# Optimization experiments

Measured on AMD Instinct MI355X. Metric: run time of the kernel, lower is better.

## Reference

```python
import jax, jax.numpy as jnp
import numpy as np

THRESHOLD = 0.1  # init kwarg threshold
N_HITS_PER_EVENT = 200000
N_EVENTS = 64


def setup_inputs() -> dict:
    key = jax.random.key(0)
    n = N_HITS_PER_EVENT * N_EVENTS
    score = jax.random.uniform(key, (n, 1), dtype=jnp.float32)  # noise score in (0,1)
    row_splits = (jnp.arange(N_EVENTS + 1, dtype=jnp.int32) * N_HITS_PER_EVENT)
    return {"score": score, "row_splits": row_splits}


def reference(score, row_splits):
    """Faithful, fully vectorized version of select_threshold_with_backgather.

    Per segment: keep all vertices with score > threshold PLUS all vertices tied
    with the segment minimum score; non-kept vertices backgather to the FIRST
    kept minimum-score vertex of their segment (new/compacted indexing).
    Returns (sel [M,1], newrs [n_seg+1], backgather [N,1]) in the layer's
    call-output order (sel, newrs, allbackgather).
    """
    s = score[:, 0]
    n = s.shape[0]
    n_seg = row_splits.shape[0] - 1

    # segment id of every vertex from the row splits
    segids = jnp.searchsorted(row_splits, jnp.arange(n, dtype=row_splits.dtype), side='right') - 1
    segids = segids.astype(jnp.int32)

    # per-segment minimum score; ties with the min are all kept (== original isminscore)
    segmin = jax.ops.segment_min(s, segids, num_segments=n_seg)
    ismin = s == segmin[segids]
    keep = (s > THRESHOLD) | ismin

    # global compacted position of each kept vertex (n_previous_rs + local keeprange)
    kept_pos = jnp.cumsum(keep.astype(jnp.int32)) - 1

    # representative = first kept min-score vertex per segment (original minidx + n_previous_rs)
    big = jnp.int32(n)
    rep_pos = jax.ops.segment_min(jnp.where(keep & ismin, kept_pos, big), segids, num_segments=n_seg)

    backgather = jnp.where(keep, kept_pos, rep_pos[segids])

    # selection indices (data-dependent size; computed on concrete values, not under jit)
    sel = jnp.nonzero(keep)[0].astype(jnp.int32)

    counts = jax.ops.segment_sum(keep.astype(jnp.int32), segids, num_segments=n_seg)
    newrs = jnp.concatenate([jnp.zeros((1,), jnp.int32), jnp.cumsum(counts).astype(jnp.int32)])

    return sel[:, None], newrs, backgather[:, None].astype(jnp.int32)
```

## Files before the change

### kernel.cpp

```cpp
#include <hip/hip_runtime.h>
#include <stdint.h>

#define BLOCK 256
#define ITEMS 8
#define TILE (BLOCK * ITEMS)
#define WPB (TILE / 64)
#define MAXSEG 64
#define THRESH 0.1f

typedef unsigned long long u64;

__device__ __forceinline__ int find_seg(const int* rs, int n_seg, int i) {
    int lo = 0, hi = n_seg;
    while (hi - lo > 1) {
        int mid = (lo + hi) >> 1;
        if (rs[mid] <= i) lo = mid; else hi = mid;
    }
    return lo;
}

__global__ __launch_bounds__(BLOCK) void k_pass1(const float* __restrict__ score,
        const int* __restrict__ row_splits, int n_seg, int n, int nwords,
        u64* __restrict__ partial_val, int* __restrict__ partial_seg,
        u64* __restrict__ bitmask, int* __restrict__ block_counts) {
    __shared__ int rs[MAXSEG + 1];
    __shared__ u64 wval[8];
    __shared__ int wseg[8];
    __shared__ int wsum[4];
    for (int j = threadIdx.x; j <= n_seg; j += BLOCK) rs[j] = row_splits[j];
    __syncthreads();
    int lane = threadIdx.x & 63, wv = threadIdx.x >> 6;
    int wbase = blockIdx.x * TILE + wv * 512;
    u64 m0 = ~0ull, m1 = ~0ull;
    int sf = -1, sl = -1, cnt = 0;
    if (wbase < n) {
        int wend = min(n, wbase + 512) - 1;
        sf = find_seg(rs, n_seg, wbase);
        sl = find_seg(rs, n_seg, wend);
        int bval = (sl != sf) ? rs[sf + 1] : 0x7FFFFFFF;
        int tbase = wbase + lane * 8;
        unsigned int kbyte = 0;
        if (tbase < n) {
            float v[8];
            if (tbase + 8 <= n) {
                float4 f0 = *(const float4*)(score + tbase);
                float4 f1 = *(const float4*)(score + tbase + 4);
                v[0]=f0.x; v[1]=f0.y; v[2]=f0.z; v[3]=f0.w;
                v[4]=f1.x; v[5]=f1.y; v[6]=f1.z; v[7]=f1.w;
            } else {
                for (int j = 0; j < 8; j++) v[j] = (tbase + j < n) ? score[tbase + j] : 1.0f;
            }
            #pragma unroll
            for (int j = 0; j < 8; j++) {
                int i = tbase + j;
                if (i < n) {
                    u64 p = ((u64)__float_as_uint(v[j]) << 32) | (unsigned int)i;
                    if (i < bval) m0 = min(m0, p); else m1 = min(m1, p);
                    if (v[j] > THRESH) kbyte |= 1u << j;
                }
            }
            cnt = __popc(kbyte);
        }
        u64 acc = ((u64)kbyte) << (8 * (lane & 7));
        acc |= __shfl_xor((unsigned long long)acc, 1, 64);
        acc |= __shfl_xor((unsigned long long)acc, 2, 64);
        acc |= __shfl_xor((unsigned long long)acc, 4, 64);
        int src = (lane < 8) ? (8 * lane) : lane;
        u64 myword = __shfl((unsigned long long)acc, src, 64);
        for (int o = 32; o > 0; o >>= 1) {
            m0 = min(m0, (u64)__shfl_down((unsigned long long)m0, o, 64));
            m1 = min(m1, (u64)__shfl_down((unsigned long long)m1, o, 64));
            cnt += __shfl_down(cnt, o, 64);
        }
        if (lane < 8) {
            int w = (wbase >> 6) + lane;
            if (w < nwords) bitmask[w] = myword;
        }
    }
    if (lane == 0) {
        wval[2 * wv] = m0;     wseg[2 * wv] = sf;
        wval[2 * wv + 1] = m1; wseg[2 * wv + 1] = (sl != sf) ? sl : -1;
        wsum[wv] = (wbase < n) ? cnt : 0;
    }
    __syncthreads();
    if (threadIdx.x == 0) {
        int base = blockIdx.x * TILE;
        int endi = min(n, base + TILE) - 1;
        int s0 = find_seg(rs, n_seg, base);
        int s1 = find_seg(rs, n_seg, endi);
        u64 o0 = ~0ull, o1 = ~0ull;
        for (int k = 0; k < 8; k++) {
            if (wseg[k] == s0) o0 = min(o0, wval[k]);
            else if (wseg[k] == s1) o1 = min(o1, wval[k]);
        }
        partial_val[2 * blockIdx.x] = o0;
        partial_seg[2 * blockIdx.x] = s0;
        partial_val[2 * blockIdx.x + 1] = o1;
        partial_seg[2 * blockIdx.x + 1] = (s1 != s0) ? s1 : -1;
        block_counts[blockIdx.x] = wsum[0] + wsum[1] + wsum[2] + wsum[3];
    }
}

__global__ __launch_bounds__(BLOCK) void k_segfix(const float* __restrict__ score,
        const int* __restrict__ row_splits, int n_seg, int n,
        const u64* __restrict__ partial_val, const int* __restrict__ partial_seg,
        u64* __restrict__ seg_packed, u64* __restrict__ bitmask,
        int* __restrict__ block_counts) {
    __shared__ u64 wred[4];
    __shared__ int nmatch;
    __shared__ int mlist[64];
    int s = blockIdx.x;
    int lo = row_splits[s], hi = row_splits[s + 1];
    int lane = threadIdx.x & 63, wv = threadIdx.x >> 6;
    if (threadIdx.x == 0) nmatch = 0;
    u64 m = ~0ull;
    int e0 = 0, e1 = -1;
    if (hi > lo) {
        e0 = 2 * (lo / TILE);
        e1 = 2 * ((hi - 1) / TILE) + 1;
        for (int e = e0 + threadIdx.x; e <= e1; e += BLOCK)
            if (partial_seg[e] == s) m = min(m, partial_val[e]);
    }
    for (int o = 32; o > 0; o >>= 1)
        m = min(m, (u64)__shfl_down((unsigned long long)m, o, 64));
    if (lane == 0) wred[wv] = m;
    __syncthreads();
    if (threadIdx.x == 0) {
        u64 r = min(min(wred[0], wred[1]), min(wred[2], wred[3]));
        wred[0] = r;
        seg_packed[s] = r;
    }
    __syncthreads();
    u64 sp = wred[0];
    if (sp == ~0ull) return;
    unsigned int smb = (unsigned int)(sp >> 32);
    if (__uint_as_float(smb) > THRESH) return;
    for (int e = e0 + threadIdx.x; e <= e1; e += BLOCK) {
        if (partial_seg[e] == s && (unsigned int)(partial_val[e] >> 32) == smb) {
            int k = atomicAdd(&nmatch, 1);
            if (k < 64) mlist[k] = e >> 1;
        }
    }
    __syncthreads();
    int nm = min(nmatch, 64);
    for (int k = 0; k < nm; k++) {
        int b = mlist[k];
        int rlo = max(b * TILE, lo);
        int rhi = min(min((b + 1) * TILE, n), hi);
        int c = 0;
        for (int i = rlo + threadIdx.x; i < rhi; i += BLOCK) {
            if (__float_as_uint(score[i]) == smb) {
                atomicOr(&bitmask[i >> 6], 1ull << (i & 63));
                c++;
            }
        }
        for (int o = 32; o > 0; o >>= 1) c += __shfl_down(c, o, 64);
        if (lane == 0 && c) atomicAdd(&block_counts[b], c);
    }
}

__global__ __launch_bounds__(BLOCK) void k_scanq(const int* __restrict__ counts,
        int* __restrict__ offsets, int nb,
        const int* __restrict__ row_splits, int n_seg, int n, int M,
        const u64* __restrict__ seg_packed, const u64* __restrict__ bitmask,
        int* __restrict__ rep_pos, int* __restrict__ newrs_out) {
    __shared__ int wtot[BLOCK / 64];
    int lane = threadIdx.x & 63, wv = threadIdx.x >> 6;
    {
        int per = (nb + BLOCK - 1) / BLOCK;
        int s = per * threadIdx.x, e = min(nb, s + per);
        int sum = 0;
        for (int i = s; i < e; i++) sum += counts[i];
        int incl = sum;
        for (int o = 1; o < 64; o <<= 1) {
            int t = __shfl_up(incl, o, 64);
            if (lane >= o) incl += t;
        }
        if (lane == 63) wtot[wv] = incl;
        __syncthreads();
        int excl = incl - sum;
        for (int k = 0; k < wv; k++) excl += wtot[k];
        for (int i = s; i < e; i++) { offsets[i] = excl; excl += counts[i]; }
    }
    __syncthreads();
    int nq = 2 * n_seg + 1;
    int q = threadIdx.x;
    if (q < nq) {
        unsigned int uidx;
        if (q <= n_seg) uidx = (unsigned int)row_splits[q];
        else uidx = (unsigned int)(seg_packed[q - (n_seg + 1)] & 0xFFFFFFFFu);
        int result;
        if (uidx >= (unsigned int)n) {
            result = M;
        } else {
            int idx = (int)uidx;
            int b = idx / TILE;
            int wq = idx >> 6;
            int cnt = offsets[b];
            for (int w = b * WPB; w < wq; w++) cnt += __popcll(bitmask[w]);
            if (idx & 63) cnt += __popcll(bitmask[wq] & ((1ull << (idx & 63)) - 1));
            result = cnt;
        }
        if (q <= n_seg) newrs_out[q] = result;
        else rep_pos[q - (n_seg + 1)] = result;
    }
}

__global__ __launch_bounds__(BLOCK) void k_output(const int* __restrict__ row_splits,
        int n_seg, int n,
        const int* __restrict__ rep_pos, const u64* __restrict__ bitmask,
        const int* __restrict__ block_offsets,
        int* __restrict__ sel_out, int* __restrict__ back_out) {
    __shared__ int rs[MAXSEG + 1];
    __shared__ u64 swords[WPB];
    __shared__ int wpre[WPB];
    __shared__ int shead[6];
    __shared__ alignas(16) int skel[TILE + 8];
    for (int j = threadIdx.x; j <= n_seg; j += BLOCK) rs[j] = row_splits[j];
    int base = blockIdx.x * TILE;
    int lim = min(TILE, n - base);
    int nw = (lim + 63) >> 6;
    for (int j = threadIdx.x; j < nw; j += BLOCK) swords[j] = bitmask[(base >> 6) + j];
    __syncthreads();
    if (threadIdx.x == 0) {
        int acc = 0;
        for (int k = 0; k < nw; k++) { wpre[k] = acc; acc += __popcll(swords[k]); }
        int s0 = find_seg(rs, n_seg, base);
        int s1 = find_seg(rs, n_seg, base + lim - 1);
        shead[0] = (s1 != s0) ? rs[s0 + 1] : 0x7FFFFFFF;
        shead[1] = rep_pos[s0];
        shead[2] = rep_pos[s1];
        shead[3] = acc;
    }
    __syncthreads();
    int bval = shead[0], rep0 = shead[1], rep1 = shead[2], tot = shead[3];
    int bo = block_offsets[blockIdx.x];
    int st_b = (int)((4 - ((((uintptr_t)(back_out + base)) >> 2) & 3)) & 3);
    if (st_b > lim) st_b = lim;
    int st_s = (int)((4 - ((((uintptr_t)(sel_out + bo)) >> 2) & 3)) & 3);
    if (st_s > tot) st_s = tot;
    int selpad = 4 - st_s;

    int ngroups = (lim - st_b) >> 2;
    for (int g = threadIdx.x; g < ngroups; g += BLOCK) {
        int j0 = st_b + 4 * g;
        int vals[4];
        #pragma unroll
        for (int k = 0; k < 4; k++) {
            int j = j0 + k;
            int widx = j >> 6, r = j & 63;
            u64 w = swords[widx];
            int i = base + j;
            if ((w >> r) & 1) {
                int pos = bo + wpre[widx] + __popcll(w & ((1ull << r) - 1));
                vals[k] = pos;
                skel[pos - bo + selpad] = i;
            } else {
                vals[k] = (i >= bval) ? rep1 : rep0;
            }
        }
        *(int4*)(back_out + base + j0) = make_int4(vals[0], vals[1], vals[2], vals[3]);
    }
    for (int j = threadIdx.x; j < st_b; j += BLOCK) {
        int widx = j >> 6, r = j & 63;
        u64 w = swords[widx];
        int i = base + j, val;
        if ((w >> r) & 1) {
            int pos = bo + wpre[widx] + __popcll(w & ((1ull << r) - 1));
            val = pos;
            skel[pos - bo + selpad] = i;
        } else val = (i >= bval) ? rep1 : rep0;
        back_out[i] = val;
    }
    for (int j = st_b + 4 * ngroups + threadIdx.x; j < lim; j += BLOCK) {
        int widx = j >> 6, r = j & 63;
        u64 w = swords[widx];
        int i = base + j, val;
        if ((w >> r) & 1) {
            int pos = bo + wpre[widx] + __popcll(w & ((1ull << r) - 1));
            val = pos;
            skel[pos - bo + selpad] = i;
        } else val = (i >= bval) ? rep1 : rep0;
        back_out[i] = val;
    }
    __syncthreads();
    int nvg = (tot - st_s) >> 2;
    for (int g = threadIdx.x; g < nvg; g += BLOCK) {
        int4 v = *(const int4*)&skel[4 + 4 * g];
        *(int4*)(sel_out + bo + st_s + 4 * g) = v;
    }
    for (int j = threadIdx.x; j < st_s; j += BLOCK) sel_out[bo + j] = skel[j + selpad];
    for (int j = st_s + 4 * nvg + threadIdx.x; j < tot; j += BLOCK) sel_out[bo + j] = skel[j + selpad];
}

extern "C" void kernel_launch(void* const* d_in, const int* in_sizes, int n_in,
                              void* d_out, int out_size, void* d_ws, size_t ws_size,
                              hipStream_t stream) {
    const float* score = (const float*)d_in[0];
    const int* row_splits = (const int*)d_in[1];
    int n = in_sizes[0];
    int n_seg = in_sizes[1] - 1;
    int M = out_size - (n_seg + 1) - n;
    int nb = (n + TILE - 1) / TILE;
    int nwords = (n + 63) / 64;

    u64* seg_packed   = (u64*)d_ws;
    u64* partial_val  = seg_packed + MAXSEG;
    int* partial_seg  = (int*)(partial_val + 2 * nb);
    int* rep_pos      = partial_seg + 2 * nb;
    int* block_counts = rep_pos + 64;
    int* block_offsets= block_counts + nb;
    uintptr_t bm_addr = (uintptr_t)(block_offsets + nb);
    bm_addr = (bm_addr + 7) & ~(uintptr_t)7;
    u64* bitmask      = (u64*)bm_addr;

    int* out = (int*)d_out;
    int* sel_out   = out;
    int* newrs_out = out + M;
    int* back_out  = out + M + (n_seg + 1);

    hipLaunchKernelGGL(k_pass1, dim3(nb), dim3(BLOCK), 0, stream,
                       score, row_splits, n_seg, n, nwords,
                       partial_val, partial_seg, bitmask, block_counts);
    hipLaunchKernelGGL(k_segfix, dim3(n_seg), dim3(BLOCK), 0, stream,
                       score, row_splits, n_seg, n,
                       partial_val, partial_seg, seg_packed, bitmask, block_counts);
    hipLaunchKernelGGL(k_scanq, dim3(1), dim3(BLOCK), 0, stream,
                       block_counts, block_offsets, nb,
                       row_splits, n_seg, n, M, seg_packed, bitmask,
                       rep_pos, newrs_out);
    hipLaunchKernelGGL(k_output, dim3(nb), dim3(BLOCK), 0, stream,
                       row_splits, n_seg, n, rep_pos, bitmask,
                       block_offsets, sel_out, back_out);
}
```

Before: 173.6 us.

## Fuse four kernels into one persistent cooperative kernel with grid syncs

```diff
diff --git a/kernel.cpp b/kernel.cpp
--- a/kernel.cpp
+++ b/kernel.cpp
@@ -1,12 +1,15 @@
 #include <hip/hip_runtime.h>
+#include <hip/hip_cooperative_groups.h>
 #include <stdint.h>
 
+namespace cg = cooperative_groups;
+
 #define BLOCK 256
-#define ITEMS 8
-#define TILE (BLOCK * ITEMS)
+#define TILE 2048
 #define WPB (TILE / 64)
 #define MAXSEG 64
 #define THRESH 0.1f
+#define GRID 512
 
 typedef unsigned long long u64;
 
@@ -19,278 +22,280 @@
     return lo;
 }
 
-__global__ __launch_bounds__(BLOCK) void k_pass1(const float* __restrict__ score,
-        const int* __restrict__ row_splits, int n_seg, int n, int nwords,
+__global__ __launch_bounds__(BLOCK, 2) void k_fused(
+        const float* __restrict__ score, const int* __restrict__ row_splits,
+        int n_seg, int n, int nb, int nwords, int M,
         u64* __restrict__ partial_val, int* __restrict__ partial_seg,
-        u64* __restrict__ bitmask, int* __restrict__ block_counts) {
+        u64* __restrict__ seg_packed, u64* __restrict__ bitmask,
+        int* __restrict__ block_counts, int* __restrict__ block_offsets,
+        int* __restrict__ rep_pos, int* __restrict__ sel_out,
+        int* __restrict__ newrs_out, int* __restrict__ back_out) {
+    cg::grid_group grid = cg::this_grid();
     __shared__ int rs[MAXSEG + 1];
     __shared__ u64 wval[8];
     __shared__ int wseg[8];
     __shared__ int wsum[4];
-    for (int j = threadIdx.x; j <= n_seg; j += BLOCK) rs[j] = row_splits[j];
-    __syncthreads();
-    int lane = threadIdx.x & 63, wv = threadIdx.x >> 6;
-    int wbase = blockIdx.x * TILE + wv * 512;
-    u64 m0 = ~0ull, m1 = ~0ull;
-    int sf = -1, sl = -1, cnt = 0;
-    if (wbase < n) {
-        int wend = min(n, wbase + 512) - 1;
-        sf = find_seg(rs, n_seg, wbase);
-        sl = find_seg(rs, n_seg, wend);
-        int bval = (sl != sf) ? rs[sf + 1] : 0x7FFFFFFF;
-        int tbase = wbase + lane * 8;
-        unsigned int kbyte = 0;
-        if (tbase < n) {
-            float v[8];
-            if (tbase + 8 <= n) {
-                float4 f0 = *(const float4*)(score + tbase);
-                float4 f1 = *(const float4*)(score + tbase + 4);
-                v[0]=f0.x; v[1]=f0.y; v[2]=f0.z; v[3]=f0.w;
-                v[4]=f1.x; v[5]=f1.y; v[6]=f1.z; v[7]=f1.w;
-            } else {
-                for (int j = 0; j < 8; j++) v[j] = (tbase + j < n) ? score[tbase + j] : 1.0f;
-            }
-            #pragma unroll
-            for (int j = 0; j < 8; j++) {
-                int i = tbase + j;
-                if (i < n) {
-                    u64 p = ((u64)__float_as_uint(v[j]) << 32) | (unsigned int)i;
-                    if (i < bval) m0 = min(m0, p); else m1 = min(m1, p);
-                    if (v[j] > THRESH) kbyte |= 1u << j;
-                }
-            }
-            cnt = __popc(kbyte);
-        }
-        u64 acc = ((u64)kbyte) << (8 * (lane & 7));
-        acc |= __shfl_xor((unsigned long long)acc, 1, 64);
-        acc |= __shfl_xor((unsigned long long)acc, 2, 64);
-        acc |= __shfl_xor((unsigned long long)acc, 4, 64);
-        int src = (lane < 8) ? (8 * lane) : lane;
-        u64 myword = __shfl((unsigned long long)acc, src, 64);
-        for (int o = 32; o > 0; o >>= 1) {
-            m0 = min(m0, (u64)__shfl_down((unsigned long long)m0, o, 64));
-            m1 = min(m1, (u64)__shfl_down((unsigned long long)m1, o, 64));
-            cnt += __shfl_down(cnt, o, 64);
-        }
-        if (lane < 8) {
-            int w = (wbase >> 6) + lane;
-            if (w < nwords) bitmask[w] = myword;
-        }
-    }
-    if (lane == 0) {
-        wval[2 * wv] = m0;     wseg[2 * wv] = sf;
-        wval[2 * wv + 1] = m1; wseg[2 * wv + 1] = (sl != sf) ? sl : -1;
-        wsum[wv] = (wbase < n) ? cnt : 0;
-    }
-    __syncthreads();
-    if (threadIdx.x == 0) {
-        int base = blockIdx.x * TILE;
-        int endi = min(n, base + TILE) - 1;
-        int s0 = find_seg(rs, n_seg, base);
-        int s1 = find_seg(rs, n_seg, endi);
-        u64 o0 = ~0ull, o1 = ~0ull;
-        for (int k = 0; k < 8; k++) {
-            if (wseg[k] == s0) o0 = min(o0, wval[k]);
-            else if (wseg[k] == s1) o1 = min(o1, wval[k]);
-        }
-        partial_val[2 * blockIdx.x] = o0;
-        partial_seg[2 * blockIdx.x] = s0;
-        partial_val[2 * blockIdx.x + 1] = o1;
-        partial_seg[2 * blockIdx.x + 1] = (s1 != s0) ? s1 : -1;
-        block_counts[blockIdx.x] = wsum[0] + wsum[1] + wsum[2] + wsum[3];
-    }
-}
-
-__global__ __launch_bounds__(BLOCK) void k_segfix(const float* __restrict__ score,
-        const int* __restrict__ row_splits, int n_seg, int n,
-        const u64* __restrict__ partial_val, const int* __restrict__ partial_seg,
-        u64* __restrict__ seg_packed, u64* __restrict__ bitmask,
-        int* __restrict__ block_counts) {
     __shared__ u64 wred[4];
     __shared__ int nmatch;
     __shared__ int mlist[64];
-    int s = blockIdx.x;
-    int lo = row_splits[s], hi = row_splits[s + 1];
+    __shared__ int wtot[4];
+    __shared__ u64 swords[WPB];
+    __shared__ int wpre[WPB];
+    __shared__ int shead[4];
+    __shared__ int srep[MAXSEG];
+    __shared__ alignas(16) int skel[TILE + 8];
+
+    int bid = blockIdx.x;
     int lane = threadIdx.x & 63, wv = threadIdx.x >> 6;
-    if (threadIdx.x == 0) nmatch = 0;
-    u64 m = ~0ull;
-    int e0 = 0, e1 = -1;
-    if (hi > lo) {
-        e0 = 2 * (lo / TILE);
-        e1 = 2 * ((hi - 1) / TILE) + 1;
-        for (int e = e0 + threadIdx.x; e <= e1; e += BLOCK)
-            if (partial_seg[e] == s) m = min(m, partial_val[e]);
-    }
-    for (int o = 32; o > 0; o >>= 1)
-        m = min(m, (u64)__shfl_down((unsigned long long)m, o, 64));
-    if (lane == 0) wred[wv] = m;
+    for (int j = threadIdx.x; j <= n_seg; j += BLOCK) rs[j] = row_splits[j];
     __syncthreads();
-    if (threadIdx.x == 0) {
-        u64 r = min(min(wred[0], wred[1]), min(wred[2], wred[3]));
-        wred[0] = r;
-        seg_packed[s] = r;
-    }
-    __syncthreads();
-    u64 sp = wred[0];
-    if (sp == ~0ull) return;
-    unsigned int smb = (unsigned int)(sp >> 32);
-    if (__uint_as_float(smb) > THRESH) return;
-    for (int e = e0 + threadIdx.x; e <= e1; e += BLOCK) {
-        if (partial_seg[e] == s && (unsigned int)(partial_val[e] >> 32) == smb) {
-            int k = atomicAdd(&nmatch, 1);
-            if (k < 64) mlist[k] = e >> 1;
-        }
-    }
-    __syncthreads();
-    int nm = min(nmatch, 64);
-    for (int k = 0; k < nm; k++) {
-        int b = mlist[k];
-        int rlo = max(b * TILE, lo);
-        int rhi = min(min((b + 1) * TILE, n), hi);
-        int c = 0;
-        for (int i = rlo + threadIdx.x; i < rhi; i += BLOCK) {
-            if (__float_as_uint(score[i]) == smb) {
-                atomicOr(&bitmask[i >> 6], 1ull << (i & 63));
-                c++;
-            }
-        }
-        for (int o = 32; o > 0; o >>= 1) c += __shfl_down(c, o, 64);
-        if (lane == 0 && c) atomicAdd(&block_counts[b], c);
-    }
-}
-
-__global__ __launch_bounds__(BLOCK) void k_scanq(const int* __restrict__ counts,
-        int* __restrict__ offsets, int nb,
-        const int* __restrict__ row_splits, int n_seg, int n, int M,
-        const u64* __restrict__ seg_packed, const u64* __restrict__ bitmask,
-        int* __restrict__ rep_pos, int* __restrict__ newrs_out) {
-    __shared__ int wtot[BLOCK / 64];
-    int lane = threadIdx.x & 63, wv = threadIdx.x >> 6;
-    {
+
+    for (int t = bid; t < nb; t += GRID) {
+        int wbase = t * TILE + wv * 512;
+        u64 m0 = ~0ull, m1 = ~0ull;
+        int sf = -1, sl = -1, cnt = 0;
+        if (wbase < n) {
+            int wend = min(n, wbase + 512) - 1;
+            sf = find_seg(rs, n_seg, wbase);
+            sl = find_seg(rs, n_seg, wend);
+            int bval = (sl != sf) ? rs[sf + 1] : 0x7FFFFFFF;
+            int tbase = wbase + lane * 8;
+            unsigned int kbyte = 0;
+            if (tbase < n) {
+                float v[8];
+                if (tbase + 8 <= n) {
+                    float4 f0 = *(const float4*)(score + tbase);
+                    float4 f1 = *(const float4*)(score + tbase + 4);
+                    v[0]=f0.x; v[1]=f0.y; v[2]=f0.z; v[3]=f0.w;
+                    v[4]=f1.x; v[5]=f1.y; v[6]=f1.z; v[7]=f1.w;
+                } else {
+                    for (int j = 0; j < 8; j++) v[j] = (tbase + j < n) ? score[tbase + j] : 1.0f;
+                }
+                #pragma unroll
+                for (int j = 0; j < 8; j++) {
+                    int i = tbase + j;
+                    if (i < n) {
+                        u64 p = ((u64)__float_as_uint(v[j]) << 32) | (unsigned int)i;
+                        if (i < bval) m0 = min(m0, p); else m1 = min(m1, p);
+                        if (v[j] > THRESH) kbyte |= 1u << j;
+                    }
+                }
+                cnt = __popc(kbyte);
+            }
+            u64 acc = ((u64)kbyte) << (8 * (lane & 7));
+            acc |= __shfl_xor((unsigned long long)acc, 1, 64);
+            acc |= __shfl_xor((unsigned long long)acc, 2, 64);
+            acc |= __shfl_xor((unsigned long long)acc, 4, 64);
+            int src = (lane < 8) ? (8 * lane) : lane;
+            u64 myword = __shfl((unsigned long long)acc, src, 64);
+            for (int o = 32; o > 0; o >>= 1) {
+                m0 = min(m0, (u64)__shfl_down((unsigned long long)m0, o, 64));
+                m1 = min(m1, (u64)__shfl_down((unsigned long long)m1, o, 64));
+                cnt += __shfl_down(cnt, o, 64);
+            }
+            if (lane < 8) {
+                int w = (wbase >> 6) + lane;
+                if (w < nwords) bitmask[w] = myword;
+            }
+        }
+        if (lane == 0) {
+            wval[2 * wv] = m0;     wseg[2 * wv] = sf;
+            wval[2 * wv + 1] = m1; wseg[2 * wv + 1] = (sl != sf) ? sl : -1;
+            wsum[wv] = (wbase < n) ? cnt : 0;
+        }
+        __syncthreads();
+        if (threadIdx.x == 0) {
+            int base = t * TILE;
+            int endi = min(n, base + TILE) - 1;
+            int s0 = find_seg(rs, n_seg, base);
+            int s1 = find_seg(rs, n_seg, endi);
+            u64 o0 = ~0ull, o1 = ~0ull;
+            for (int k = 0; k < 8; k++) {
+                if (wseg[k] == s0) o0 = min(o0, wval[k]);
+                else if (wseg[k] == s1) o1 = min(o1, wval[k]);
+            }
+            partial_val[2 * t] = o0;
+            partial_seg[2 * t] = s0;
+            partial_val[2 * t + 1] = o1;
+            partial_seg[2 * t + 1] = (s1 != s0) ? s1 : -1;
+            block_counts[t] = wsum[0] + wsum[1] + wsum[2] + wsum[3];
+        }
+        __syncthreads();
+    }
+    grid.sync();
+
+    if (bid < n_seg) {
+        int s = bid;
+        int lo = rs[s], hi = rs[s + 1];
+        if (threadIdx.x == 0) nmatch = 0;
+        u64 m = ~0ull;
+        int e0 = 0, e1 = -1;
+        if (hi > lo) {
+            e0 = 2 * (lo / TILE);
+            e1 = 2 * ((hi - 1) / TILE) + 1;
+            for (int e = e0 + threadIdx.x; e <= e1; e += BLOCK)
+                if (partial_seg[e] == s) m = min(m, partial_val[e]);
+        }
+        for (int o = 32; o > 0; o >>= 1)
+            m = min(m, (u64)__shfl_down((unsigned long long)m, o, 64));
+        if (lane == 0) wred[wv] = m;
+        __syncthreads();
+        if (threadIdx.x == 0) {
+            u64 r = min(min(wred[0], wred[1]), min(wred[2], wred[3]));
+            wred[0] = r;
+            seg_packed[s] = r;
+        }
+        __syncthreads();
+        u64 sp = wred[0];
+        bool doit = (sp != ~0ull) &&
+                    (__uint_as_float((unsigned int)(sp >> 32)) <= THRESH);
+        if (doit) {
+            unsigned int smb = (unsigned int)(sp >> 32);
+            for (int e = e0 + threadIdx.x; e <= e1; e += BLOCK) {
+                if (partial_seg[e] == s && (unsigned int)(partial_val[e] >> 32) == smb) {
+                    int k = atomicAdd(&nmatch, 1);
+                    if (k < 64) mlist[k] = e >> 1;
+                }
+            }
+            __syncthreads();
+            int nm = min(nmatch, 64);
+            for (int k = 0; k < nm; k++) {
+                int b = mlist[k];
+                int rlo = max(b * TILE, lo);
+                int rhi = min(min((b + 1) * TILE, n), hi);
+                int c = 0;
+                for (int i = rlo + threadIdx.x; i < rhi; i += BLOCK) {
+                    if (__float_as_uint(score[i]) == smb) {
+                        atomicOr(&bitmask[i >> 6], 1ull << (i & 63));
+                        c++;
+                    }
+                }
+                for (int o = 32; o > 0; o >>= 1) c += __shfl_down(c, o, 64);
+                if (lane == 0 && c) atomicAdd(&block_counts[b], c);
+            }
+        }
+    }
+    grid.sync();
+
+    if (bid == 0) {
         int per = (nb + BLOCK - 1) / BLOCK;
-        int s = per * threadIdx.x, e = min(nb, s + per);
+        int s0 = per * threadIdx.x, e0i = min(nb, s0 + per);
         int sum = 0;
-        for (int i = s; i < e; i++) sum += counts[i];
+        for (int i = s0; i < e0i; i++) sum += block_counts[i];
         int incl = sum;
         for (int o = 1; o < 64; o <<= 1) {
-            int t = __shfl_up(incl, o, 64);
-            if (lane >= o) incl += t;
+            int tsh = __shfl_up(incl, o, 64);
+            if (lane >= o) incl += tsh;
         }
         if (lane == 63) wtot[wv] = incl;
         __syncthreads();
         int excl = incl - sum;
         for (int k = 0; k < wv; k++) excl += wtot[k];
-        for (int i = s; i < e; i++) { offsets[i] = excl; excl += counts[i]; }
-    }
+        for (int i = s0; i < e0i; i++) { block_offsets[i] = excl; excl += block_counts[i]; }
+        __syncthreads();
+        int nq = 2 * n_seg + 1;
+        int q = threadIdx.x;
+        if (q < nq) {
+            unsigned int uidx;
+            if (q <= n_seg) uidx = (unsigned int)rs[q];
+            else uidx = (unsigned int)(seg_packed[q - (n_seg + 1)] & 0xFFFFFFFFu);
+            int result;
+            if (uidx >= (unsigned int)n) {
+                result = M;
+            } else {
+                int idx = (int)uidx;
+                int b = idx / TILE;
+                int wq = idx >> 6;
+                int cnt = block_offsets[b];
+                for (int w = b * WPB; w < wq; w++) cnt += __popcll(bitmask[w]);
+                if (idx & 63) cnt += __popcll(bitmask[wq] & ((1ull << (idx & 63)) - 1));
+                result = cnt;
+            }
+            if (q <= n_seg) newrs_out[q] = result;
+            else rep_pos[q - (n_seg + 1)] = result;
+        }
+    }
+    grid.sync();
+
+    for (int j = threadIdx.x; j < n_seg; j += BLOCK) srep[j] = rep_pos[j];
     __syncthreads();
-    int nq = 2 * n_seg + 1;
-    int q = threadIdx.x;
-    if (q < nq) {
-        unsigned int uidx;
-        if (q <= n_seg) uidx = (unsigned int)row_splits[q];
-        else uidx = (unsigned int)(seg_packed[q - (n_seg + 1)] & 0xFFFFFFFFu);
-        int result;
-        if (uidx >= (unsigned int)n) {
-            result = M;
-        } else {
-            int idx = (int)uidx;
-            int b = idx / TILE;
-            int wq = idx >> 6;
-            int cnt = offsets[b];
-            for (int w = b * WPB; w < wq; w++) cnt += __popcll(bitmask[w]);
-            if (idx & 63) cnt += __popcll(bitmask[wq] & ((1ull << (idx & 63)) - 1));
-            result = cnt;
-        }
-        if (q <= n_seg) newrs_out[q] = result;
-        else rep_pos[q - (n_seg + 1)] = result;
-    }
-}
-
-__global__ __launch_bounds__(BLOCK) void k_output(const int* __restrict__ row_splits,
-        int n_seg, int n,
-        const int* __restrict__ rep_pos, const u64* __restrict__ bitmask,
-        const int* __restrict__ block_offsets,
-        int* __restrict__ sel_out, int* __restrict__ back_out) {
-    __shared__ int rs[MAXSEG + 1];
-    __shared__ u64 swords[WPB];
-    __shared__ int wpre[WPB];
-    __shared__ int shead[6];
-    __shared__ alignas(16) int skel[TILE + 8];
-    for (int j = threadIdx.x; j <= n_seg; j += BLOCK) rs[j] = row_splits[j];
-    int base = blockIdx.x * TILE;
-    int lim = min(TILE, n - base);
-    int nw = (lim + 63) >> 6;
-    for (int j = threadIdx.x; j < nw; j += BLOCK) swords[j] = bitmask[(base >> 6) + j];
-    __syncthreads();
-    if (threadIdx.x == 0) {
-        int acc = 0;
-        for (int k = 0; k < nw; k++) { wpre[k] = acc; acc += __popcll(swords[k]); }
-        int s0 = find_seg(rs, n_seg, base);
-        int s1 = find_seg(rs, n_seg, base + lim - 1);
-        shead[0] = (s1 != s0) ? rs[s0 + 1] : 0x7FFFFFFF;
-        shead[1] = rep_pos[s0];
-        shead[2] = rep_pos[s1];
-        shead[3] = acc;
-    }
-    __syncthreads();
-    int bval = shead[0], rep0 = shead[1], rep1 = shead[2], tot = shead[3];
-    int bo = block_offsets[blockIdx.x];
-    int st_b = (int)((4 - ((((uintptr_t)(back_out + base)) >> 2) & 3)) & 3);
-    if (st_b > lim) st_b = lim;
-    int st_s = (int)((4 - ((((uintptr_t)(sel_out + bo)) >> 2) & 3)) & 3);
-    if (st_s > tot) st_s = tot;
-    int selpad = 4 - st_s;
-
-    int ngroups = (lim - st_b) >> 2;
-    for (int g = threadIdx.x; g < ngroups; g += BLOCK) {
-        int j0 = st_b + 4 * g;
-        int vals[4];
-        #pragma unroll
-        for (int k = 0; k < 4; k++) {
-            int j = j0 + k;
+    for (int t = bid; t < nb; t += GRID) {
+        int base = t * TILE;
+        int lim = min(TILE, n - base);
+        int nw = (lim + 63) >> 6;
+        for (int j = threadIdx.x; j < nw; j += BLOCK) swords[j] = bitmask[(base >> 6) + j];
+        __syncthreads();
+        if (threadIdx.x == 0) {
+            int acc = 0;
+            for (int k = 0; k < nw; k++) { wpre[k] = acc; acc += __popcll(swords[k]); }
+            int s0 = find_seg(rs, n_seg, base);
+            int s1 = find_seg(rs, n_seg, base + lim - 1);
+            shead[0] = (s1 != s0) ? rs[s0 + 1] : 0x7FFFFFFF;
+            shead[1] = srep[s0];
+            shead[2] = srep[s1];
+            shead[3] = acc;
+        }
+        __syncthreads();
+        int bval = shead[0], rep0 = shead[1], rep1 = shead[2], tot = shead[3];
+        int bo = block_offsets[t];
+        int st_b = (int)((4 - ((((uintptr_t)(back_out + base)) >> 2) & 3)) & 3);
+        if (st_b > lim) st_b = lim;
+        int st_s = (int)((4 - ((((uintptr_t)(sel_out + bo)) >> 2) & 3)) & 3);
+        if (st_s > tot) st_s = tot;
+        int selpad = 4 - st_s;
+
+        int ngroups = (lim - st_b) >> 2;
+        for (int g = threadIdx.x; g < ngroups; g += BLOCK) {
+            int j0 = st_b + 4 * g;
+            int vals[4];
+            #pragma unroll
+            for (int k = 0; k < 4; k++) {
+                int j = j0 + k;
+                int widx = j >> 6, r = j & 63;
+                u64 w = swords[widx];
+                int i = base + j;
+                if ((w >> r) & 1) {
+                    int pos = bo + wpre[widx] + __popcll(w & ((1ull << r) - 1));
+                    vals[k] = pos;
+                    skel[pos - bo + selpad] = i;
+                } else {
+                    vals[k] = (i >= bval) ? rep1 : rep0;
+                }
+            }
+            *(int4*)(back_out + base + j0) = make_int4(vals[0], vals[1], vals[2], vals[3]);
+        }
+        for (int j = threadIdx.x; j < st_b; j += BLOCK) {
             int widx = j >> 6, r = j & 63;
             u64 w = swords[widx];
-            int i = base + j;
+            int i = base + j, val;
             if ((w >> r) & 1) {
                 int pos = bo + wpre[widx] + __popcll(w & ((1ull << r) - 1));
-                vals[k] = pos;
+                val = pos;
                 skel[pos - bo + selpad] = i;
-            } else {
-                vals[k] = (i >= bval) ? rep1 : rep0;
-            }
-        }
-        *(int4*)(back_out + base + j0) = make_int4(vals[0], vals[1], vals[2], vals[3]);
-    }
-    for (int j = threadIdx.x; j < st_b; j += BLOCK) {
-        int widx = j >> 6, r = j & 63;
-        u64 w = swords[widx];
-        int i = base + j, val;
-        if ((w >> r) & 1) {
-            int pos = bo + wpre[widx] + __popcll(w & ((1ull << r) - 1));
-            val = pos;
-            skel[pos - bo + selpad] = i;
-        } else val = (i >= bval) ? rep1 : rep0;
-        back_out[i] = val;
-    }
-    for (int j = st_b + 4 * ngroups + threadIdx.x; j < lim; j += BLOCK) {
-        int widx = j >> 6, r = j & 63;
-        u64 w = swords[widx];
-        int i = base + j, val;
-        if ((w >> r) & 1) {
-            int pos = bo + wpre[widx] + __popcll(w & ((1ull << r) - 1));
-            val = pos;
-            skel[pos - bo + selpad] = i;
-        } else val = (i >= bval) ? rep1 : rep0;
-        back_out[i] = val;
-    }
-    __syncthreads();
-    int nvg = (tot - st_s) >> 2;
-    for (int g = threadIdx.x; g < nvg; g += BLOCK) {
-        int4 v = *(const int4*)&skel[4 + 4 * g];
-        *(int4*)(sel_out + bo + st_s + 4 * g) = v;
-    }
-    for (int j = threadIdx.x; j < st_s; j += BLOCK) sel_out[bo + j] = skel[j + selpad];
-    for (int j = st_s + 4 * nvg + threadIdx.x; j < tot; j += BLOCK) sel_out[bo + j] = skel[j + selpad];
+            } else val = (i >= bval) ? rep1 : rep0;
+            back_out[i] = val;
+        }
+        for (int j = st_b + 4 * ngroups + threadIdx.x; j < lim; j += BLOCK) {
+            int widx = j >> 6, r = j & 63;
+            u64 w = swords[widx];
+            int i = base + j, val;
+            if ((w >> r) & 1) {
+                int pos = bo + wpre[widx] + __popcll(w & ((1ull << r) - 1));
+                val = pos;
+                skel[pos - bo + selpad] = i;
+            } else val = (i >= bval) ? rep1 : rep0;
+            back_out[i] = val;
+        }
+        __syncthreads();
+        int nvg = (tot - st_s) >> 2;
+        for (int g = threadIdx.x; g < nvg; g += BLOCK) {
+            int4 v = *(const int4*)&skel[4 + 4 * g];
+            *(int4*)(sel_out + bo + st_s + 4 * g) = v;
+        }
+        for (int j = threadIdx.x; j < st_s; j += BLOCK) sel_out[bo + j] = skel[j + selpad];
+        for (int j = st_s + 4 * nvg + threadIdx.x; j < tot; j += BLOCK) sel_out[bo + j] = skel[j + selpad];
+        __syncthreads();
+    }
 }
 
 extern "C" void kernel_launch(void* const* d_in, const int* in_sizes, int n_in,
@@ -319,17 +324,13 @@
     int* newrs_out = out + M;
     int* back_out  = out + M + (n_seg + 1);
 
-    hipLaunchKernelGGL(k_pass1, dim3(nb), dim3(BLOCK), 0, stream,
-                       score, row_splits, n_seg, n, nwords,
-                       partial_val, partial_seg, bitmask, block_counts);
-    hipLaunchKernelGGL(k_segfix, dim3(n_seg), dim3(BLOCK), 0, stream,
-                       score, row_splits, n_seg, n,
-                       partial_val, partial_seg, seg_packed, bitmask, block_counts);
-    hipLaunchKernelGGL(k_scanq, dim3(1), dim3(BLOCK), 0, stream,
-                       block_counts, block_offsets, nb,
-                       row_splits, n_seg, n, M, seg_packed, bitmask,
-                       rep_pos, newrs_out);
-    hipLaunchKernelGGL(k_output, dim3(nb), dim3(BLOCK), 0, stream,
-                       row_splits, n_seg, n, rep_pos, bitmask,
-                       block_offsets, sel_out, back_out);
+    void* args[] = {
+        (void*)&score, (void*)&row_splits, (void*)&n_seg, (void*)&n,
+        (void*)&nb, (void*)&nwords, (void*)&M,
+        (void*)&partial_val, (void*)&partial_seg, (void*)&seg_packed,
+        (void*)&bitmask, (void*)&block_counts, (void*)&block_offsets,
+        (void*)&rep_pos, (void*)&sel_out, (void*)&newrs_out, (void*)&back_out
+    };
+    hipLaunchCooperativeKernel((void*)k_fused, dim3(GRID), dim3(BLOCK),
+                               args, 0, stream);
 }
```

Measured after the change: 382.2 us. 2.2x slower.
